# Performance work log

Hardware: AMD Instinct MI355X
Metric: run time of the kernel (lower is better)

## Reference

```python
import jax, jax.numpy as jnp
import numpy as np

B, T = 2048, 8192


def setup_inputs() -> dict:
    key = jax.random.key(0)
    k1, k2, k3, k4 = jax.random.split(key, 4)
    return {
        "target_angle": jax.random.normal(k1, (B, T), dtype=jnp.float32),
        "target_class": jax.random.normal(k2, (B, 3), dtype=jnp.float32),
        "pred_angle": jax.random.normal(k3, (B, T), dtype=jnp.float32),
        "pred_class": jax.random.normal(k4, (B, 3), dtype=jnp.float32),
    }


def reference(target_angle, target_class, pred_angle, pred_class):
    # score_angle: WMA(target) - WMA(pred) == WMA(target - pred) since WMA is linear.
    # Padding 2 zeros per side + 5-tap valid correlation yields T output positions,
    # exactly matching the original python loop over range(T+4-4).
    w = jnp.asarray([0.05, 0.1, 0.7, 0.1, 0.05], dtype=target_angle.dtype)
    diff = target_angle - pred_angle                       # [B, T]
    dp = jnp.pad(diff, ((0, 0), (2, 2)))                   # [B, T+4]
    t = diff.shape[1]
    # 5-term fused sum instead of per-position slice loop
    wma = (w[0] * dp[:, 0:t] + w[1] * dp[:, 1:t + 1] + w[2] * dp[:, 2:t + 2]
           + w[3] * dp[:, 3:t + 3] + w[4] * dp[:, 4:t + 4])  # [B, T]
    d_angle = jnp.sum(wma * wma)

    # score_class: sum of squared errors over the first 3 class columns
    dc = target_class[:, :3] - pred_class[:, :3]
    d_class = jnp.sum(dc * dc)

    return d_angle * 0.8 + d_class * 0.2
```

## Files before the change

### kernel.cpp

```cpp
#include <hip/hip_runtime.h>


#define NTHREADS 256
#define PER_THREAD 8

__global__ __launch_bounds__(NTHREADS) void wma_partial_kernel(
    const float* __restrict__ ta, const float* __restrict__ pa,
    float* __restrict__ partial, int T)
{
    const int t = threadIdx.x;
    const long e = ((long)blockIdx.x * NTHREADS + t) * PER_THREAD;
    const int col = (int)(e % T);

    const float4* ta4 = (const float4*)(ta + e);
    const float4* pa4 = (const float4*)(pa + e);
    const float4 a0 = ta4[0], a1 = ta4[1];
    const float4 p0 = pa4[0], p1 = pa4[1];

    const float d0 = a0.x - p0.x, d1 = a0.y - p0.y, d2 = a0.z - p0.z, d3 = a0.w - p0.w;
    const float d4 = a1.x - p1.x, d5 = a1.y - p1.y, d6 = a1.z - p1.z, d7 = a1.w - p1.w;

    const int lane = t & 63;
    float dm2 = __shfl_up(d6, 1, 64);
    float dm1 = __shfl_up(d7, 1, 64);
    float dp8 = __shfl_down(d0, 1, 64);
    float dp9 = __shfl_down(d1, 1, 64);

    if (lane == 0) {
        dm1 = (col >= 1) ? (ta[e - 1] - pa[e - 1]) : 0.0f;
        dm2 = (col >= 2) ? (ta[e - 2] - pa[e - 2]) : 0.0f;
    }
    if (lane == 63) {
        dp8 = (col + PER_THREAD     < T) ? (ta[e + 8] - pa[e + 8]) : 0.0f;
        dp9 = (col + PER_THREAD + 1 < T) ? (ta[e + 9] - pa[e + 9]) : 0.0f;
    }

    float acc = 0.0f, w;
    w = 0.05f*dm2 + 0.1f*dm1 + 0.7f*d0 + 0.1f*d1  + 0.05f*d2;  acc += w*w;
    w = 0.05f*dm1 + 0.1f*d0  + 0.7f*d1 + 0.1f*d2  + 0.05f*d3;  acc += w*w;
    w = 0.05f*d0  + 0.1f*d1  + 0.7f*d2 + 0.1f*d3  + 0.05f*d4;  acc += w*w;
    w = 0.05f*d1  + 0.1f*d2  + 0.7f*d3 + 0.1f*d4  + 0.05f*d5;  acc += w*w;
    w = 0.05f*d2  + 0.1f*d3  + 0.7f*d4 + 0.1f*d5  + 0.05f*d6;  acc += w*w;
    w = 0.05f*d3  + 0.1f*d4  + 0.7f*d5 + 0.1f*d6  + 0.05f*d7;  acc += w*w;
    w = 0.05f*d4  + 0.1f*d5  + 0.7f*d6 + 0.1f*d7  + 0.05f*dp8; acc += w*w;
    w = 0.05f*d5  + 0.1f*d6  + 0.7f*d7 + 0.1f*dp8 + 0.05f*dp9; acc += w*w;

#pragma unroll
    for (int off = 32; off; off >>= 1) acc += __shfl_down(acc, off, 64);

    __shared__ float wsum[NTHREADS / 64];
    if ((t & 63) == 0) wsum[t >> 6] = acc;
    __syncthreads();
    if (t == 0) {
        float b = 0.0f;
#pragma unroll
        for (int i = 0; i < NTHREADS / 64; ++i) b += wsum[i];
        partial[blockIdx.x] = b;
    }
}

__global__ __launch_bounds__(NTHREADS) void finalize_kernel(
    const float* __restrict__ partial, int nPartial,
    const float* __restrict__ tc, const float* __restrict__ pc, int nClass,
    float* __restrict__ out)
{
    const int t = threadIdx.x;

    float sa = 0.0f;
    for (int i = t; i < nPartial; i += NTHREADS) sa += partial[i];

    float sc = 0.0f;
    for (int i = t; i < nClass; i += NTHREADS) {
        const float d = tc[i] - pc[i];
        sc += d * d;
    }

#pragma unroll
    for (int off = 32; off; off >>= 1) {
        sa += __shfl_down(sa, off, 64);
        sc += __shfl_down(sc, off, 64);
    }

    __shared__ float ra[NTHREADS / 64], rc[NTHREADS / 64];
    if ((t & 63) == 0) { ra[t >> 6] = sa; rc[t >> 6] = sc; }
    __syncthreads();
    if (t == 0) {
        float a = 0.0f, c = 0.0f;
#pragma unroll
        for (int i = 0; i < NTHREADS / 64; ++i) { a += ra[i]; c += rc[i]; }
        out[0] = 0.8f * a + 0.2f * c;
    }
}

extern "C" void kernel_launch(void* const* d_in, const int* in_sizes, int n_in,
                              void* d_out, int out_size, void* d_ws, size_t ws_size,
                              hipStream_t stream)
{
    const float* ta = (const float*)d_in[0];
    const float* tc = (const float*)d_in[1];
    const float* pa = (const float*)d_in[2];
    const float* pc = (const float*)d_in[3];
    float* out = (float*)d_out;

    const int nAngle = in_sizes[0];
    const int nClass = in_sizes[1];
    const int T = 8192;
    const int grid = nAngle / (NTHREADS * PER_THREAD);

    float* partial = (float*)d_ws;

    wma_partial_kernel<<<grid, NTHREADS, 0, stream>>>(ta, pa, partial, T);
    finalize_kernel<<<1, NTHREADS, 0, stream>>>(partial, grid, tc, pc, nClass, out);
}
```

Baseline: 43.12 us.

## Assign one row per block with four batched segments per thread

Each block now processes a full row of 8192 elements, with each thread loading four 8-element segments up front before computing. The grid shrinks from 8192 to 2048 blocks, and the finalize kernel reduces four times fewer partials. The goal is more memory-level parallelism per thread and less per-block launch and reduction overhead. The cost is higher register pressure and fewer waves to hide latency.

```diff
diff --git a/kernel.cpp b/kernel.cpp
--- a/kernel.cpp
+++ b/kernel.cpp
@@ -2,48 +2,73 @@
 
 
 #define NTHREADS 256
-#define PER_THREAD 8
+#define SEGS 4
+#define SEGSPAN (NTHREADS * 8)
 
 __global__ __launch_bounds__(NTHREADS) void wma_partial_kernel(
     const float* __restrict__ ta, const float* __restrict__ pa,
     float* __restrict__ partial, int T)
 {
     const int t = threadIdx.x;
-    const long e = ((long)blockIdx.x * NTHREADS + t) * PER_THREAD;
-    const int col = (int)(e % T);
+    const int lane = t & 63;
+    const long rowBase = (long)blockIdx.x * T;
 
-    const float4* ta4 = (const float4*)(ta + e);
-    const float4* pa4 = (const float4*)(pa + e);
-    const float4 a0 = ta4[0], a1 = ta4[1];
-    const float4 p0 = pa4[0], p1 = pa4[1];
-
-    const float d0 = a0.x - p0.x, d1 = a0.y - p0.y, d2 = a0.z - p0.z, d3 = a0.w - p0.w;
-    const float d4 = a1.x - p1.x, d5 = a1.y - p1.y, d6 = a1.z - p1.z, d7 = a1.w - p1.w;
-
-    const int lane = t & 63;
-    float dm2 = __shfl_up(d6, 1, 64);
-    float dm1 = __shfl_up(d7, 1, 64);
-    float dp8 = __shfl_down(d0, 1, 64);
-    float dp9 = __shfl_down(d1, 1, 64);
-
-    if (lane == 0) {
-        dm1 = (col >= 1) ? (ta[e - 1] - pa[e - 1]) : 0.0f;
-        dm2 = (col >= 2) ? (ta[e - 2] - pa[e - 2]) : 0.0f;
-    }
-    if (lane == 63) {
-        dp8 = (col + PER_THREAD     < T) ? (ta[e + 8] - pa[e + 8]) : 0.0f;
-        dp9 = (col + PER_THREAD + 1 < T) ? (ta[e + 9] - pa[e + 9]) : 0.0f;
+    float4 A[SEGS][2], P[SEGS][2];
+#pragma unroll
+    for (int s = 0; s < SEGS; ++s) {
+        const long e = rowBase + (long)s * SEGSPAN + (long)t * 8;
+        const float4* ta4 = (const float4*)(ta + e);
+        const float4* pa4 = (const float4*)(pa + e);
+        A[s][0] = ta4[0]; A[s][1] = ta4[1];
+        P[s][0] = pa4[0]; P[s][1] = pa4[1];
     }
 
-    float acc = 0.0f, w;
-    w = 0.05f*dm2 + 0.1f*dm1 + 0.7f*d0 + 0.1f*d1  + 0.05f*d2;  acc += w*w;
-    w = 0.05f*dm1 + 0.1f*d0  + 0.7f*d1 + 0.1f*d2  + 0.05f*d3;  acc += w*w;
-    w = 0.05f*d0  + 0.1f*d1  + 0.7f*d2 + 0.1f*d3  + 0.05f*d4;  acc += w*w;
-    w = 0.05f*d1  + 0.1f*d2  + 0.7f*d3 + 0.1f*d4  + 0.05f*d5;  acc += w*w;
-    w = 0.05f*d2  + 0.1f*d3  + 0.7f*d4 + 0.1f*d5  + 0.05f*d6;  acc += w*w;
-    w = 0.05f*d3  + 0.1f*d4  + 0.7f*d5 + 0.1f*d6  + 0.05f*d7;  acc += w*w;
-    w = 0.05f*d4  + 0.1f*d5  + 0.7f*d6 + 0.1f*d7  + 0.05f*dp8; acc += w*w;
-    w = 0.05f*d5  + 0.1f*d6  + 0.7f*d7 + 0.1f*dp8 + 0.05f*dp9; acc += w*w;
+    float em2[SEGS], em1[SEGS], ep8[SEGS], ep9[SEGS];
+#pragma unroll
+    for (int s = 0; s < SEGS; ++s) { em2[s] = em1[s] = ep8[s] = ep9[s] = 0.0f; }
+#pragma unroll
+    for (int s = 0; s < SEGS; ++s) {
+        const int col = s * SEGSPAN + t * 8;
+        const long e = rowBase + col;
+        if (lane == 0) {
+            if (col >= 1) em1[s] = ta[e - 1] - pa[e - 1];
+            if (col >= 2) em2[s] = ta[e - 2] - pa[e - 2];
+        }
+        if (lane == 63) {
+            if (col + 8 < T) ep8[s] = ta[e + 8] - pa[e + 8];
+            if (col + 9 < T) ep9[s] = ta[e + 9] - pa[e + 9];
+        }
+    }
+
+    float acc = 0.0f;
+#pragma unroll
+    for (int s = 0; s < SEGS; ++s) {
+        const float d0 = A[s][0].x - P[s][0].x;
+        const float d1 = A[s][0].y - P[s][0].y;
+        const float d2 = A[s][0].z - P[s][0].z;
+        const float d3 = A[s][0].w - P[s][0].w;
+        const float d4 = A[s][1].x - P[s][1].x;
+        const float d5 = A[s][1].y - P[s][1].y;
+        const float d6 = A[s][1].z - P[s][1].z;
+        const float d7 = A[s][1].w - P[s][1].w;
+
+        float dm2 = __shfl_up(d6, 1, 64);
+        float dm1 = __shfl_up(d7, 1, 64);
+        float dp8 = __shfl_down(d0, 1, 64);
+        float dp9 = __shfl_down(d1, 1, 64);
+        if (lane == 0)  { dm2 = em2[s]; dm1 = em1[s]; }
+        if (lane == 63) { dp8 = ep8[s]; dp9 = ep9[s]; }
+
+        float w;
+        w = 0.05f*dm2 + 0.1f*dm1 + 0.7f*d0 + 0.1f*d1  + 0.05f*d2;  acc += w*w;
+        w = 0.05f*dm1 + 0.1f*d0  + 0.7f*d1 + 0.1f*d2  + 0.05f*d3;  acc += w*w;
+        w = 0.05f*d0  + 0.1f*d1  + 0.7f*d2 + 0.1f*d3  + 0.05f*d4;  acc += w*w;
+        w = 0.05f*d1  + 0.1f*d2  + 0.7f*d3 + 0.1f*d4  + 0.05f*d5;  acc += w*w;
+        w = 0.05f*d2  + 0.1f*d3  + 0.7f*d4 + 0.1f*d5  + 0.05f*d6;  acc += w*w;
+        w = 0.05f*d3  + 0.1f*d4  + 0.7f*d5 + 0.1f*d6  + 0.05f*d7;  acc += w*w;
+        w = 0.05f*d4  + 0.1f*d5  + 0.7f*d6 + 0.1f*d7  + 0.05f*dp8; acc += w*w;
+        w = 0.05f*d5  + 0.1f*d6  + 0.7f*d7 + 0.1f*dp8 + 0.05f*dp9; acc += w*w;
+    }
 
 #pragma unroll
     for (int off = 32; off; off >>= 1) acc += __shfl_down(acc, off, 64);
@@ -105,10 +130,10 @@
     const int nAngle = in_sizes[0];
     const int nClass = in_sizes[1];
     const int T = 8192;
-    const int grid = nAngle / (NTHREADS * PER_THREAD);
+    const int B = nAngle / T;
 
     float* partial = (float*)d_ws;
 
-    wma_partial_kernel<<<grid, NTHREADS, 0, stream>>>(ta, pa, partial, T);
-    finalize_kernel<<<1, NTHREADS, 0, stream>>>(partial, grid, tc, pc, nClass, out);
+    wma_partial_kernel<<<B, NTHREADS, 0, stream>>>(ta, pa, partial, T);
+    finalize_kernel<<<1, NTHREADS, 0, stream>>>(partial, B, tc, pc, nClass, out);
 }
```

New measurement: 40.91 us. -5.1%, faster.
